# Kernel optimization log

Measured on AMD Instinct MI355X. Metric: run time of the kernel, lower is better.

The kernel has to match this reference:

```python
import jax, jax.numpy as jnp
import numpy as np
from jax import lax

V_TH = 1.0  # spiking threshold (spikingjelly default)

# Heaviside spike with Rect surrogate gradient (width 1 around threshold)
@jax.custom_vjp
def spike(v):
    return (v >= V_TH).astype(v.dtype)

def _spike_fwd(v):
    return spike(v), v

def _spike_bwd(v, g):
    return (g * (jnp.abs(v - V_TH) < 0.5).astype(g.dtype),)

spike.defvjp(_spike_fwd, _spike_bwd)


def synapse_filter(x, inv_tau):
    # y[t] = y[t-1] * (1 - inv_tau) + x[t]   (spikingjelly SynapseFilter)
    decay = 1.0 - inv_tau
    def step(y, xt):
        y = y * decay + xt
        return y, y
    _, ys = lax.scan(step, jnp.zeros_like(x[0]), x)
    return ys


def lif_seq(x, tau):
    # LIFNode, decay_input=True, v_reset=0 (hard reset): v += (x - v)/tau
    inv_tau = 1.0 / tau
    def step(v, xt):
        v = v + (xt - v) * inv_tau
        s = spike(v)
        return v * (1.0 - s), s
    _, ss = lax.scan(step, jnp.zeros_like(x[0]), x)
    return ss


def if_seq(x):
    # IFNode, v_reset=0 (hard reset): v += x
    def step(v, xt):
        v = v + xt
        s = spike(v)
        return v * (1.0 - s), s
    _, ss = lax.scan(step, jnp.zeros_like(x[0]), x)
    return ss


def setup_inputs() -> dict:
    key = jax.random.key(0)
    ks = jax.random.split(key, 12)
    T, N, C, A = 32, 64, 512, 32
    F = [2048, 1024, 512]
    f32 = jnp.float32

    def lin_w(k, out_d, in_d):
        b = 1.0 / np.sqrt(in_d)
        return jax.random.uniform(k, (out_d, in_d), f32, -b, b)

    x = jax.random.uniform(ks[0], (T, N, 2, C), f32)  # (T,N,2,C) input currents
    w_sf_init = jnp.asarray(-np.log(10.0 - 1.0), f32)  # sigmoid(w)=1/tau, tau=10
    return {
        "x": x,
        "w_jeff": lin_w(ks[1], A, 2),        # JeffressLinear weight: 2 -> cc_acc
        "w_cc": lin_w(ks[2], 1, A),          # Linear(cc_acc, 1)
        "w_sf0": w_sf_init,
        "W1": lin_w(ks[3], F[0], C),
        "w_sf1": w_sf_init,
        "W2": lin_w(ks[4], F[1], F[0]),
        "w_sf2": w_sf_init,
        "W3": lin_w(ks[5], F[2], F[1]),
        "w_sf3": w_sf_init,
        "W_out": lin_w(ks[6], 1, F[2]),
        "b_out": jax.random.uniform(ks[7], (1,), f32, -1.0 / np.sqrt(F[2]), 1.0 / np.sqrt(F[2])),
    }


def reference(x, w_jeff, w_cc, w_sf0, W1, w_sf1, W2, w_sf2, W3, w_sf3, W_out, b_out):
    JEFF_TAU = 2.0
    LIF_TAU = 1.5
    # TransposeLayer((2,3)): (T,N,2,C) -> (T,N,C,2)
    y = jnp.swapaxes(x, 2, 3)
    # JeffressLinear(cc_acc, tau=2, bias=False): synapse low-pass then 2 -> cc_acc
    y = synapse_filter(y, 1.0 / JEFF_TAU)
    y = jnp.einsum('tnci,ai->tnca', y, w_jeff)
    # LIFNode(tau=1.5)
    y = lif_seq(y, LIF_TAU)
    # SynapseFilter(tau=10, learnable)
    y = synapse_filter(y, jax.nn.sigmoid(w_sf0))
    # Linear(cc_acc, 1) + Flatten(start_dim=2): (T,N,C,A) -> (T,N,C)
    y = jnp.einsum('tnca,oa->tnco', y, w_cc)[..., 0]
    # IFNode
    y = if_seq(y)
    # stacked [SynapseFilter, Linear, IFNode] blocks
    for w_sf, W in ((w_sf1, W1), (w_sf2, W2), (w_sf3, W3)):
        y = synapse_filter(y, jax.nn.sigmoid(w_sf))
        y = jnp.einsum('tnc,oc->tno', y, W)
        y = if_seq(y)
    # final Linear(feature_dims[-1], 1, bias=True)
    y = jnp.einsum('tnf,of->tno', y, W_out) + b_out
    # NonSpikingIFNode: v[t] = v[t-1] + x[t], output membrane potential
    out = jnp.cumsum(y, axis=0)  # (T, N, 1)
    return out
```

## Files before the change

kernel.cpp:

```cpp
#include <hip/hip_runtime.h>
#include <math.h>

#define T_STEPS 32
#define NB 64
#define CC 512
#define AA 32
#define MROWS (T_STEPS * NB)

typedef __attribute__((ext_vector_type(8)))  short bf16x8;
typedef __attribute__((ext_vector_type(16))) float f32x16;

__device__ __forceinline__ float sig_decay(const float* wp) {
    return 1.0f - 1.0f / (1.0f + expf(-wp[0]));
}

__device__ __forceinline__ unsigned short f2bf_rne(float f) {
    unsigned int u = __float_as_uint(f);
    u += 0x7FFF + ((u >> 16) & 1);
    return (unsigned short)(u >> 16);
}


#define NW1 (2048 * 512)
#define NW2 (1024 * 2048)
#define NW3 (512 * 1024)

__device__ __forceinline__ void pack_one(
    const float* __restrict__ W, unsigned short* __restrict__ out,
    int idx, int Nw, int Kw, int kshift)
{
    int n = idx >> kshift;
    int k = idx & (Kw - 1);
    float w = W[idx];
    unsigned short h = f2bf_rne(w);
    float fh = __uint_as_float((unsigned int)h << 16);
    float r = w - fh;
    unsigned short m = f2bf_rne(r);
    float fm = __uint_as_float((unsigned int)m << 16);
    unsigned short l = f2bf_rne(r - fm);
    unsigned short vals[3] = {h, m, l};
    const int NT = Nw >> 5, KS = Kw >> 4;
    int L = (n & 31) + 32 * ((k >> 3) & 1);
#pragma unroll
    for (int p = 0; p < 3; p++) {
        size_t chunk = ((size_t)(p * NT + (n >> 5)) * KS + (k >> 4)) * 64 + L;
        out[chunk * 8 + (k & 7)] = vals[p];
    }
}

__global__ __launch_bounds__(256) void pack_all_kernel(
    const float* __restrict__ W1, const float* __restrict__ W2,
    const float* __restrict__ W3,
    unsigned short* __restrict__ B1, unsigned short* __restrict__ B2,
    unsigned short* __restrict__ B3)
{
    int i = blockIdx.x * 256 + threadIdx.x;
    if (i < NW1) {
        pack_one(W1, B1, i, 2048, 512, 9);
    } else if (i < NW1 + NW2) {
        pack_one(W2, B2, i - NW1, 1024, 2048, 11);
    } else if (i < NW1 + NW2 + NW3) {
        pack_one(W3, B3, i - NW1 - NW2, 512, 1024, 10);
    }
}

__global__ __launch_bounds__(256) void front_kernel(
    const float* __restrict__ x, const float* __restrict__ w_jeff,
    const float* __restrict__ w_cc, const float* __restrict__ w_sf0,
    const float* __restrict__ w_sf1,
    unsigned short* __restrict__ spike_out, float* __restrict__ filt_out)
{
    __shared__ float wj[2 * AA];
    __shared__ float wcc[AA];
    int tid = threadIdx.x;
    if (tid < 2 * AA) wj[tid] = w_jeff[tid];
    if (tid < AA) wcc[tid] = w_cc[tid];
    __syncthreads();

    int g = blockIdx.x * 256 + tid;
    int n = g >> 9;
    int c = g & (CC - 1);

    const float inv_lif = 1.0f / 1.5f;
    float d0 = sig_decay(w_sf0);
    float d1 = sig_decay(w_sf1);

    float s0 = 0.f, s1 = 0.f, v6 = 0.f, u1 = 0.f;
    float v[AA], u[AA];
#pragma unroll
    for (int a = 0; a < AA; a++) { v[a] = 0.f; u[a] = 0.f; }

    const int pL = (n & 31) + 32 * ((c >> 3) & 1);
    const int pks = c >> 4;
    const int pj = c & 7;

    for (int t = 0; t < T_STEPS; t++) {
        const float* xp = x + (size_t)((t * NB + n) * 2) * CC + c;
        s0 = s0 * 0.5f + xp[0];
        s1 = s1 * 0.5f + xp[CC];
        float acc = 0.f;
#pragma unroll
        for (int a = 0; a < AA; a++) {
            float z  = wj[2 * a] * s0 + wj[2 * a + 1] * s1;
            float vv = v[a] + (z - v[a]) * inv_lif;
            bool  sp = vv >= 1.0f;
            v[a] = sp ? 0.0f : vv;
            float uu = u[a] * d0 + (sp ? 1.0f : 0.0f);
            u[a] = uu;
            acc += wcc[a] * uu;
        }
        v6 += acc;
        bool sp6 = v6 >= 1.0f;
        v6 = sp6 ? 0.0f : v6;
        if (spike_out) {
            int mt = (t * NB + n) >> 5;
            size_t adr = (((size_t)mt * 32 + pks) * 64 + pL) * 8 + pj;
            spike_out[adr] = sp6 ? (unsigned short)0x3F80 : (unsigned short)0;
        } else {
            u1 = u1 * d1 + (sp6 ? 1.0f : 0.0f);
            filt_out[(size_t)(t * NB + n) * CC + c] = u1;
        }
    }
}

template <int NPARTS>
__global__ __launch_bounds__(256) void if_spike_kernel(
    const float* __restrict__ G, size_t partStride,
    const float* __restrict__ w_sf_in, int F, int fshift,
    unsigned short* __restrict__ out_bf, float* __restrict__ out_f32)
{
    constexpr int TT = 16 / NPARTS;
    constexpr int NTILES = T_STEPS / TT;

    int gid = blockIdx.x * 256 + threadIdx.x;
    int n = gid >> fshift;
    int f = gid & (F - 1);
    const int NT = F >> 5;
    const int NF = NB * F;
    float dz = sig_decay(w_sf_in);

    size_t base = ((size_t)(n >> 5) * NT + (f >> 5)) * 1024
                + (size_t)(n & 31) * 32 + (f & 31);
    const size_t tstride = (size_t)2 * NT * 1024;

    float buf[2][NPARTS][TT];
    auto pf = [&](int b, int tile) {
#pragma unroll
        for (int p = 0; p < NPARTS; p++)
#pragma unroll
            for (int j = 0; j < TT; j++)
                buf[b][p][j] = G[(size_t)p * partStride + base
                               + (size_t)(tile * TT + j) * tstride];
    };

    const int pL = (n & 31) + 32 * ((f >> 3) & 1);
    const int KS = F >> 4;

    pf(0, 0);
    float zf = 0.f, v = 0.f;
#pragma unroll
    for (int tile = 0; tile < NTILES; tile++) {
        const int b = tile & 1;
        if (tile + 1 < NTILES) pf(b ^ 1, tile + 1);
        __builtin_amdgcn_sched_barrier(0);
#pragma unroll
        for (int j = 0; j < TT; j++) {
            int t = tile * TT + j;
            float gsum = buf[b][0][j];
#pragma unroll
            for (int p = 1; p < NPARTS; p++) gsum += buf[b][p][j];
            zf = zf * dz + gsum;
            v += zf;
            bool sp = v >= 1.0f;
            v = sp ? 0.0f : v;
            if (out_bf) {
                int mt = 2 * t + (n >> 5);
                size_t adr = (((size_t)mt * KS + (f >> 4)) * 64 + pL) * 8 + (f & 7);
                out_bf[adr] = sp ? (unsigned short)0x3F80 : (unsigned short)0;
            } else {
                out_f32[(size_t)t * NF + gid] = sp ? 1.0f : 0.0f;
            }
        }
        __builtin_amdgcn_sched_barrier(0);
    }
}

__global__ __launch_bounds__(256, 2) void bgemm(
    const unsigned short* __restrict__ Ap,
    const unsigned short* __restrict__ Bp,
    float* __restrict__ C,
    int N, int K_total, int K_per)
{
    const int NT = N >> 5, KS = K_total >> 4;
    __shared__ bf16x8 shA[2][256];

    const int tid = threadIdx.x;
    const int wv  = tid >> 6;
    const int L   = tid & 63;
    const int bm32 = blockIdx.x * 4;
    const int bn32 = blockIdx.y * 4;
    const int ks0  = (blockIdx.z * K_per) >> 4;
    const int nk   = K_per >> 4;

    f32x16 acc[4];
#pragma unroll
    for (int i = 0; i < 4; i++)
#pragma unroll
        for (int r = 0; r < 16; r++) acc[i][r] = 0.f;

    const bf16x8* A8 = (const bf16x8*)Ap;
    const bf16x8* B8 = (const bf16x8*)Bp;

    bf16x8 pa;
    auto gloadA = [&](int ks) {
        pa = A8[((size_t)(bm32 + wv) * KS + ks) * 64 + L];
    };
    auto lwriteA = [&](int b) { shA[b][tid] = pa; };

    bf16x8 pb0[3], pb1[3];
    auto gloadB = [&](int ks, bf16x8* pbuf) {
#pragma unroll
        for (int p = 0; p < 3; p++)
            pbuf[p] = B8[((size_t)(p * NT + bn32 + wv) * KS + ks) * 64 + L];
    };

    bf16x8 af[4];
    auto rfragsA = [&](int b) {
#pragma unroll
        for (int i = 0; i < 4; i++)
            af[i] = shA[b][i * 64 + L];
    };

    gloadA(ks0);
    gloadB(ks0, pb0);
    lwriteA(0);
    gloadA(ks0 + 1);
    gloadB(ks0 + 1, pb1);
    __syncthreads();
    rfragsA(0);

#define BG_STAGE(KT, CB, PB)                                                  \
    {                                                                         \
        bf16x8 b0 = PB[0], b1 = PB[1], b2 = PB[2];                            \
        if ((KT) + 1 < nk) lwriteA((CB) ^ 1);           \
        if ((KT) + 2 < nk) {                                                  \
            gloadA(ks0 + (KT) + 2);                                           \
            gloadB(ks0 + (KT) + 2, PB);                                       \
        }                                                                     \
        _Pragma("unroll")                                                     \
        for (int i = 0; i < 4; i++)                                           \
            acc[i] = __builtin_amdgcn_mfma_f32_32x32x16_bf16(af[i], b0, acc[i], 0, 0, 0); \
        _Pragma("unroll")                                                     \
        for (int i = 0; i < 4; i++)                                           \
            acc[i] = __builtin_amdgcn_mfma_f32_32x32x16_bf16(af[i], b1, acc[i], 0, 0, 0); \
        _Pragma("unroll")                                                     \
        for (int i = 0; i < 4; i++)                                           \
            acc[i] = __builtin_amdgcn_mfma_f32_32x32x16_bf16(af[i], b2, acc[i], 0, 0, 0); \
        if ((KT) + 1 < nk) { __syncthreads(); rfragsA((CB) ^ 1); }            \
    }

    for (int kt = 0; kt < nk; kt += 2) {
        BG_STAGE(kt, 0, pb0);
        BG_STAGE(kt + 1, 1, pb1);
    }
#undef BG_STAGE

    float* Cp = C + (size_t)blockIdx.z * ((size_t)MROWS * N);
    const int col = L & 31, rbase = 4 * (L >> 5);
#pragma unroll
    for (int i = 0; i < 4; i++) {
        size_t tb = ((size_t)(bm32 + i) * NT + (bn32 + wv)) * 1024;
#pragma unroll
        for (int r = 0; r < 16; r++) {
            int row = (r & 3) + 8 * (r >> 2) + rbase;
            Cp[tb + row * 32 + col] = acc[i][r];
        }
    }
}

__global__ __launch_bounds__(256) void if_filter_kernel(
    float* __restrict__ buf, size_t partStride, int nparts,
    const float* __restrict__ w_sf, int F)
{
    int tid = blockIdx.x * 256 + threadIdx.x;
    const int NF = NB * F;
    bool  filt = (w_sf != nullptr);
    float d = filt ? sig_decay(w_sf) : 0.0f;
    float v = 0.f, u = 0.f;
    for (int t = 0; t < T_STEPS; t++) {
        size_t off = (size_t)t * NF + tid;
        float zt = buf[off];
        for (int p = 1; p < nparts; p++) zt += buf[p * partStride + off];
        v += zt;
        bool sp = v >= 1.0f;
        v = sp ? 0.0f : v;
        float s = sp ? 1.0f : 0.0f;
        if (filt) { u = u * d + s; buf[off] = u; }
        else      { buf[off] = s; }
    }
}

__global__ __launch_bounds__(256) void gemm_nt(
    const float* __restrict__ A, const float* __restrict__ B,
    float* __restrict__ C, int M, int N, int K_total, int K_per)
{
    constexpr int BM = 64, BN = 64, BK = 32;
    __shared__ float As[BK][BM + 4];
    __shared__ float Bs[BK][BN + 4];
    const int tid = threadIdx.x;
    const int tx  = tid & 15;
    const int ty  = tid >> 4;
    const int bm  = blockIdx.y * BM;
    const int bn  = blockIdx.x * BN;
    const int kbeg = blockIdx.z * K_per;
    float acc[4][4];
#pragma unroll
    for (int i = 0; i < 4; i++)
#pragma unroll
        for (int j = 0; j < 4; j++) acc[i][j] = 0.f;
    const int lrow = tid >> 3;
    const int lkq  = tid & 7;
    for (int kt = 0; kt < K_per; kt += BK) {
        int k0 = kbeg + kt;
        __syncthreads();
#pragma unroll
        for (int i = 0; i < 2; i++) {
            int row = lrow + i * 32;
            float4 av = *(const float4*)(A + (size_t)(bm + row) * K_total + k0 + lkq * 4);
            As[lkq * 4 + 0][row] = av.x;
            As[lkq * 4 + 1][row] = av.y;
            As[lkq * 4 + 2][row] = av.z;
            As[lkq * 4 + 3][row] = av.w;
            float4 bv = *(const float4*)(B + (size_t)(bn + row) * K_total + k0 + lkq * 4);
            Bs[lkq * 4 + 0][row] = bv.x;
            Bs[lkq * 4 + 1][row] = bv.y;
            Bs[lkq * 4 + 2][row] = bv.z;
            Bs[lkq * 4 + 3][row] = bv.w;
        }
        __syncthreads();
#pragma unroll
        for (int kk = 0; kk < BK; kk++) {
            float4 a0 = *(const float4*)&As[kk][ty * 4];
            float4 b0 = *(const float4*)&Bs[kk][tx * 4];
            float ar[4] = {a0.x, a0.y, a0.z, a0.w};
            float br[4] = {b0.x, b0.y, b0.z, b0.w};
#pragma unroll
            for (int i = 0; i < 4; i++)
#pragma unroll
                for (int j = 0; j < 4; j++) acc[i][j] += ar[i] * br[j];
        }
    }
    float* Cp = C + (size_t)blockIdx.z * (size_t)M * N;
#pragma unroll
    for (int i = 0; i < 4; i++) {
        float4 o;
        o.x = acc[i][0]; o.y = acc[i][1]; o.z = acc[i][2]; o.w = acc[i][3];
        *(float4*)(Cp + (size_t)(bm + ty * 4 + i) * N + bn + tx * 4) = o;
    }
}

__global__ __launch_bounds__(64) void final_kernel(
    const float* __restrict__ y15, const float* __restrict__ W_out,
    const float* __restrict__ b_out, float* __restrict__ out)
{
    int n = blockIdx.x;
    int lane = threadIdx.x;
    float w[8];
#pragma unroll
    for (int j = 0; j < 8; j++) w[j] = W_out[lane + j * 64];
    float b = b_out[0];
    float cum = 0.f;
    for (int t = 0; t < T_STEPS; t++) {
        const float* yp = y15 + (size_t)(t * NB + n) * 512;
        float p = 0.f;
#pragma unroll
        for (int j = 0; j < 8; j++) p += yp[lane + j * 64] * w[j];
#pragma unroll
        for (int off = 32; off > 0; off >>= 1) p += __shfl_down(p, off);
        if (lane == 0) {
            cum += p + b;
            out[t * NB + n] = cum;
        }
    }
}

extern "C" void kernel_launch(void* const* d_in, const int* in_sizes, int n_in,
                              void* d_out, int out_size, void* d_ws, size_t ws_size,
                              hipStream_t stream) {
    (void)in_sizes; (void)n_in; (void)out_size;
    const float* x      = (const float*)d_in[0];
    const float* w_jeff = (const float*)d_in[1];
    const float* w_cc   = (const float*)d_in[2];
    const float* w_sf0  = (const float*)d_in[3];
    const float* W1     = (const float*)d_in[4];
    const float* w_sf1  = (const float*)d_in[5];
    const float* W2     = (const float*)d_in[6];
    const float* w_sf2  = (const float*)d_in[7];
    const float* W3     = (const float*)d_in[8];
    const float* w_sf3  = (const float*)d_in[9];
    const float* W_out  = (const float*)d_in[10];
    const float* b_out  = (const float*)d_in[11];
    float* out = (float*)d_out;
    const int M = MROWS;

    const size_t nW1 = NW1, nW2 = NW2, nW3 = NW3;
    size_t need = 3 * (nW1 + nW2 + nW3) * 2
                + (size_t)M * 512 * 2
                + (size_t)2 * M * 2048 * 4
                + (size_t)M * 2048 * 2
                + (size_t)M * 1024 * 2
                + (size_t)M * 512 * 4;

    if (ws_size >= need) {
        unsigned short* Bp1 = (unsigned short*)d_ws;
        unsigned short* Bp2 = Bp1 + 3 * nW1;
        unsigned short* Bp3 = Bp2 + 3 * nW2;
        unsigned short* s6  = Bp3 + 3 * nW3;
        float* G   = (float*)(s6 + (size_t)M * 512);
        unsigned short* s8  = (unsigned short*)(G + (size_t)2 * M * 2048);
        unsigned short* s10 = s8 + (size_t)M * 2048;
        float* s12 = (float*)(s10 + (size_t)M * 1024);

        pack_all_kernel<<<(int)((nW1 + nW2 + nW3 + 255) / 256), 256, 0, stream>>>(
            W1, W2, W3, Bp1, Bp2, Bp3);

        front_kernel<<<NB * CC / 256, 256, 0, stream>>>(
            x, w_jeff, w_cc, w_sf0, w_sf1, s6, nullptr);

        bgemm<<<dim3(16, 16, 2), 256, 0, stream>>>(s6, Bp1, G, 2048, 512, 256);
        if_spike_kernel<2><<<NB * 2048 / 256, 256, 0, stream>>>(
            G, (size_t)M * 2048, w_sf1, 2048, 11, s8, nullptr);

        bgemm<<<dim3(16, 8, 4), 256, 0, stream>>>(s8, Bp2, G, 1024, 2048, 512);
        if_spike_kernel<4><<<NB * 1024 / 256, 256, 0, stream>>>(
            G, (size_t)M * 1024, w_sf2, 1024, 10, s10, nullptr);

        bgemm<<<dim3(16, 4, 8), 256, 0, stream>>>(s10, Bp3, G, 512, 1024, 128);
        if_spike_kernel<8><<<NB * 512 / 256, 256, 0, stream>>>(
            G, (size_t)M * 512, w_sf3, 512, 9, nullptr, s12);

        final_kernel<<<NB, 64, 0, stream>>>(s12, W_out, b_out, out);
    } else {
        float* y7  = (float*)d_ws;
        float* z1  = y7 + (size_t)M * 512;
        float* z2p = z1 + (size_t)M * 2048;
        float* z3p = z1;
        size_t need2 = ((size_t)M * 512 + (size_t)M * 2048 + 2 * (size_t)M * 1024) * 4;
        const int ksplit2 = (ws_size >= need2) ? 2 : 1;

        front_kernel<<<NB * CC / 256, 256, 0, stream>>>(
            x, w_jeff, w_cc, w_sf0, w_sf1, nullptr, y7);
        gemm_nt<<<dim3(2048 / 64, 2048 / 64, 1), 256, 0, stream>>>(
            y7, W1, z1, M, 2048, 512, 512);
        if_filter_kernel<<<NB * 2048 / 256, 256, 0, stream>>>(z1, 0, 1, w_sf2, 2048);
        gemm_nt<<<dim3(1024 / 64, 2048 / 64, ksplit2), 256, 0, stream>>>(
            z1, W2, z2p, M, 1024, 2048, 2048 / ksplit2);
        if_filter_kernel<<<NB * 1024 / 256, 256, 0, stream>>>(
            z2p, (size_t)M * 1024, ksplit2, w_sf3, 1024);
        gemm_nt<<<dim3(512 / 64, 2048 / 64, 4), 256, 0, stream>>>(
            z2p, W3, z3p, M, 512, 1024, 1024 / 4);
        if_filter_kernel<<<NB * 512 / 256, 256, 0, stream>>>(
            z3p, (size_t)M * 512, 4, nullptr, 512);
        final_kernel<<<NB, 64, 0, stream>>>(z3p, W_out, b_out, out);
    }
}
```

Measured before the change: 226.6 us.

## Split K inside bgemm blocks across two wave groups with LDS reduction

Measured after the change: 227.8 us. About the same (+0.5%).

```diff
diff --git a/kernel.cpp b/kernel.cpp
--- a/kernel.cpp
+++ b/kernel.cpp
@@ -185,22 +185,24 @@
     }
 }
 
-__global__ __launch_bounds__(256, 2) void bgemm(
+__global__ __launch_bounds__(512, 2) void bgemm(
     const unsigned short* __restrict__ Ap,
     const unsigned short* __restrict__ Bp,
     float* __restrict__ C,
     int N, int K_total, int K_per)
 {
     const int NT = N >> 5, KS = K_total >> 4;
-    __shared__ bf16x8 shA[2][256];
+    __shared__ bf16x8 shA[2][2][256];
 
     const int tid = threadIdx.x;
-    const int wv  = tid >> 6;
+    const int g   = tid >> 8;
+    const int lt  = tid & 255;
+    const int sn  = (tid >> 6) & 3;
     const int L   = tid & 63;
     const int bm32 = blockIdx.x * 4;
     const int bn32 = blockIdx.y * 4;
     const int ks0  = (blockIdx.z * K_per) >> 4;
-    const int nk   = K_per >> 4;
+    const int nk2  = K_per >> 5;
 
     f32x16 acc[4];
 #pragma unroll
@@ -212,40 +214,40 @@
     const bf16x8* B8 = (const bf16x8*)Bp;
 
     bf16x8 pa;
-    auto gloadA = [&](int ks) {
-        pa = A8[((size_t)(bm32 + wv) * KS + ks) * 64 + L];
+    auto gloadA = [&](int s) {
+        pa = A8[((size_t)(bm32 + (lt >> 6)) * KS + ks0 + 2 * s + g) * 64 + (lt & 63)];
     };
-    auto lwriteA = [&](int b) { shA[b][tid] = pa; };
+    auto lwriteA = [&](int b) { shA[g][b][lt] = pa; };
 
     bf16x8 pb0[3], pb1[3];
-    auto gloadB = [&](int ks, bf16x8* pbuf) {
+    auto gloadB = [&](int s, bf16x8* pbuf) {
 #pragma unroll
         for (int p = 0; p < 3; p++)
-            pbuf[p] = B8[((size_t)(p * NT + bn32 + wv) * KS + ks) * 64 + L];
+            pbuf[p] = B8[((size_t)(p * NT + bn32 + sn) * KS + ks0 + 2 * s + g) * 64 + L];
     };
 
     bf16x8 af[4];
     auto rfragsA = [&](int b) {
 #pragma unroll
         for (int i = 0; i < 4; i++)
-            af[i] = shA[b][i * 64 + L];
+            af[i] = shA[g][b][i * 64 + L];
     };
 
-    gloadA(ks0);
-    gloadB(ks0, pb0);
+    gloadA(0);
+    gloadB(0, pb0);
     lwriteA(0);
-    gloadA(ks0 + 1);
-    gloadB(ks0 + 1, pb1);
+    gloadA(1);
+    gloadB(1, pb1);
     __syncthreads();
     rfragsA(0);
 
-#define BG_STAGE(KT, CB, PB)                                                  \
+#define BG_STAGE(S, CB, PB)                                                   \
     {                                                                         \
         bf16x8 b0 = PB[0], b1 = PB[1], b2 = PB[2];                            \
-        if ((KT) + 1 < nk) lwriteA((CB) ^ 1);           \
-        if ((KT) + 2 < nk) {                                                  \
-            gloadA(ks0 + (KT) + 2);                                           \
-            gloadB(ks0 + (KT) + 2, PB);                                       \
+        if ((S) + 1 < nk2) lwriteA((CB) ^ 1);         \
+        if ((S) + 2 < nk2) {                                                  \
+            gloadA((S) + 2);                                                  \
+            gloadB((S) + 2, PB);                                              \
         }                                                                     \
         _Pragma("unroll")                                                     \
         for (int i = 0; i < 4; i++)                                           \
@@ -256,24 +258,43 @@
         _Pragma("unroll")                                                     \
         for (int i = 0; i < 4; i++)                                           \
             acc[i] = __builtin_amdgcn_mfma_f32_32x32x16_bf16(af[i], b2, acc[i], 0, 0, 0); \
-        if ((KT) + 1 < nk) { __syncthreads(); rfragsA((CB) ^ 1); }            \
-    }
-
-    for (int kt = 0; kt < nk; kt += 2) {
-        BG_STAGE(kt, 0, pb0);
-        BG_STAGE(kt + 1, 1, pb1);
+        if ((S) + 1 < nk2) { __syncthreads(); rfragsA((CB) ^ 1); }            \
+    }
+
+    for (int s = 0; s < nk2; s += 2) {
+        BG_STAGE(s, 0, pb0);
+        BG_STAGE(s + 1, 1, pb1);
     }
 #undef BG_STAGE
 
-    float* Cp = C + (size_t)blockIdx.z * ((size_t)MROWS * N);
-    const int col = L & 31, rbase = 4 * (L >> 5);
+    float* shf = (float*)shA;
 #pragma unroll
     for (int i = 0; i < 4; i++) {
-        size_t tb = ((size_t)(bm32 + i) * NT + (bn32 + wv)) * 1024;
-#pragma unroll
-        for (int r = 0; r < 16; r++) {
-            int row = (r & 3) + 8 * (r >> 2) + rbase;
-            Cp[tb + row * 32 + col] = acc[i][r];
+        __syncthreads();
+        if (g == 1) {
+#pragma unroll
+            for (int r = 0; r < 16; r++)
+                shf[sn * 1024 + r * 64 + L] = acc[i][r];
+        }
+        __syncthreads();
+        if (g == 0) {
+#pragma unroll
+            for (int r = 0; r < 16; r++)
+                acc[i][r] += shf[sn * 1024 + r * 64 + L];
+        }
+    }
+
+    if (g == 0) {
+        float* Cp = C + (size_t)blockIdx.z * ((size_t)MROWS * N);
+        const int col = L & 31, rbase = 4 * (L >> 5);
+#pragma unroll
+        for (int i = 0; i < 4; i++) {
+            size_t tb = ((size_t)(bm32 + i) * NT + (bn32 + sn)) * 1024;
+#pragma unroll
+            for (int r = 0; r < 16; r++) {
+                int row = (r & 3) + 8 * (r >> 2) + rbase;
+                Cp[tb + row * 32 + col] = acc[i][r];
+            }
         }
     }
 }
@@ -406,7 +427,7 @@
     const size_t nW1 = NW1, nW2 = NW2, nW3 = NW3;
     size_t need = 3 * (nW1 + nW2 + nW3) * 2
                 + (size_t)M * 512 * 2
-                + (size_t)2 * M * 2048 * 4
+                + (size_t)M * 2048 * 4
                 + (size_t)M * 2048 * 2
                 + (size_t)M * 1024 * 2
                 + (size_t)M * 512 * 4;
@@ -417,7 +438,7 @@
         unsigned short* Bp3 = Bp2 + 3 * nW2;
         unsigned short* s6  = Bp3 + 3 * nW3;
         float* G   = (float*)(s6 + (size_t)M * 512);
-        unsigned short* s8  = (unsigned short*)(G + (size_t)2 * M * 2048);
+        unsigned short* s8  = (unsigned short*)(G + (size_t)M * 2048);
         unsigned short* s10 = s8 + (size_t)M * 2048;
         float* s12 = (float*)(s10 + (size_t)M * 1024);
 
@@ -427,16 +448,16 @@
         front_kernel<<<NB * CC / 256, 256, 0, stream>>>(
             x, w_jeff, w_cc, w_sf0, w_sf1, s6, nullptr);
 
-        bgemm<<<dim3(16, 16, 2), 256, 0, stream>>>(s6, Bp1, G, 2048, 512, 256);
-        if_spike_kernel<2><<<NB * 2048 / 256, 256, 0, stream>>>(
-            G, (size_t)M * 2048, w_sf1, 2048, 11, s8, nullptr);
-
-        bgemm<<<dim3(16, 8, 4), 256, 0, stream>>>(s8, Bp2, G, 1024, 2048, 512);
-        if_spike_kernel<4><<<NB * 1024 / 256, 256, 0, stream>>>(
+        bgemm<<<dim3(16, 16, 1), 512, 0, stream>>>(s6, Bp1, G, 2048, 512, 512);
+        if_spike_kernel<1><<<NB * 2048 / 256, 256, 0, stream>>>(
+            G, 0, w_sf1, 2048, 11, s8, nullptr);
+
+        bgemm<<<dim3(16, 8, 2), 512, 0, stream>>>(s8, Bp2, G, 1024, 2048, 1024);
+        if_spike_kernel<2><<<NB * 1024 / 256, 256, 0, stream>>>(
             G, (size_t)M * 1024, w_sf2, 1024, 10, s10, nullptr);
 
-        bgemm<<<dim3(16, 4, 8), 256, 0, stream>>>(s10, Bp3, G, 512, 1024, 128);
-        if_spike_kernel<8><<<NB * 512 / 256, 256, 0, stream>>>(
+        bgemm<<<dim3(16, 4, 4), 512, 0, stream>>>(s10, Bp3, G, 512, 1024, 256);
+        if_spike_kernel<4><<<NB * 512 / 256, 256, 0, stream>>>(
             G, (size_t)M * 512, w_sf3, 512, 9, nullptr, s12);
 
         final_kernel<<<NB, 64, 0, stream>>>(s12, W_out, b_out, out);
```
